# Kernel tuning notes

Measured on AMD Instinct MI355X. Metric: run time of the kernel, lower is better.

The kernel has to match this reference:

```python
import jax, jax.numpy as jnp
import numpy as np

EPS_NORM = 1e-08
EPS_Q = 1e-05

def rmsnorm(x, w):
    v = jnp.mean(jnp.square(x.astype(jnp.float32)), axis=-1, keepdims=True)
    x_hat = x * jax.lax.rsqrt(v + EPS_NORM)
    return (x_hat * w).astype(x.dtype)

def activation_quant(x):
    # per-token 8-bit fake quant
    scale = 127.0 / jnp.clip(jnp.max(jnp.abs(x), axis=-1, keepdims=True), EPS_Q, None)
    return jnp.clip(jnp.round(x * scale), -128, 127) / scale

def weight_quant(w):
    # per-tensor 1.58-bit (ternary) fake quant
    scale = 1.0 / jnp.clip(jnp.mean(jnp.abs(w)), EPS_Q, None)
    return jnp.clip(jnp.round(w * scale), -1, 1) / scale

def bitlinear(x, norm_w, w):
    x_norm = rmsnorm(x, norm_w)
    x_q = x_norm + jax.lax.stop_gradient(activation_quant(x_norm) - x_norm)
    w_q = w + jax.lax.stop_gradient(weight_quant(w) - w)
    return jnp.einsum('bsd,hd->bsh', x_q, w_q)

def setup_inputs() -> dict:
    key = jax.random.key(0)
    k1, k2, k3 = jax.random.split(key, 3)
    dim, hidden = 1024, 4096
    return {
        'x': jax.random.normal(k1, (4, 2048, dim), dtype=jnp.float32),
        'norm1_w': jnp.ones((dim,), jnp.float32),
        'w1': jax.random.normal(k2, (hidden, dim), jnp.float32) * 0.02,
        'act_scale': jnp.ones((1,), jnp.float32),
        'act_bias': jnp.zeros((1,), jnp.float32),
        'norm2_w': jnp.ones((hidden,), jnp.float32),
        'w2': jax.random.normal(k3, (dim, hidden), jnp.float32) * 0.02,
    }

def reference(x, norm1_w, w1, act_scale, act_bias, norm2_w, w2):
    h = bitlinear(x, norm1_w, w1)                       # [B,S,hidden]
    h = act_scale * jnp.square(jax.nn.relu(h)) + act_bias  # StarReLU
    y = bitlinear(h, norm2_w, w2)                       # [B,S,dim]
    return y
```

## Files before the change

### kernel.cpp

```cpp
#include <hip/hip_runtime.h>
#include <stdint.h>

#define EPS_NORM 1e-8
#define EPS_Q 1e-5

typedef int v4i __attribute__((ext_vector_type(4)));

__device__ __forceinline__ double wave_sum_d(double v) {
#pragma unroll
  for (int o = 32; o; o >>= 1) v += __shfl_xor(v, o);
  return v;
}
__device__ __forceinline__ float wave_max(float v) {
#pragma unroll
  for (int o = 32; o; o >>= 1) v = fmaxf(v, __shfl_xor(v, o));
  return v;
}

__global__ void wabs_sum_kernel(const float* __restrict__ w1,
                                const float* __restrict__ w2,
                                double* __restrict__ sums) {
  const float4* w = (const float4*)(blockIdx.y ? w2 : w1);
  const int n4 = 4194304 / 4;
  double s = 0.0;
  for (int i = blockIdx.x * blockDim.x + threadIdx.x; i < n4;
       i += gridDim.x * blockDim.x) {
    float4 t = w[i];
    s += (double)fabsf(t.x) + (double)fabsf(t.y) + (double)fabsf(t.z) +
         (double)fabsf(t.w);
  }
  s = wave_sum_d(s);
  __shared__ double red[4];
  const int wid = threadIdx.x >> 6;
  if ((threadIdx.x & 63) == 0) red[wid] = s;
  __syncthreads();
  if (threadIdx.x == 0)
    atomicAdd(&sums[blockIdx.y], red[0] + red[1] + red[2] + red[3]);
}

__global__ void wquant_kernel(const float* __restrict__ w, int8_t* __restrict__ q,
                              const double* __restrict__ sum, double ninv) {
  const double s = 1.0 / fmax(sum[0] * ninv, EPS_Q);
  const int i = blockIdx.x * blockDim.x + threadIdx.x;
  float4 t = ((const float4*)w)[i];
  int a = (int)rint((double)t.x * s); a = a < -1 ? -1 : (a > 1 ? 1 : a);
  int b = (int)rint((double)t.y * s); b = b < -1 ? -1 : (b > 1 ? 1 : b);
  int c = (int)rint((double)t.z * s); c = c < -1 ? -1 : (c > 1 ? 1 : c);
  int d = (int)rint((double)t.w * s); d = d < -1 ? -1 : (d > 1 ? 1 : d);
  ((int*)q)[i] = (a & 255) | ((b & 255) << 8) | ((c & 255) << 16) | ((d & 255) << 24);
}

template <int D>
__global__ __launch_bounds__(256) void rq_kernel(
    const float* __restrict__ X, const float* __restrict__ W,
    int8_t* __restrict__ Q, float* __restrict__ recips) {
  constexpr int C = D / 1024;
  const int t = blockIdx.x;
  const int tid = threadIdx.x;
  const int wid = tid >> 6;
  const int lane = tid & 63;
  const float4* xr = (const float4*)(X + (size_t)t * D);
  const float4* wr = (const float4*)W;
  float4 xv[C];
  double ss = 0.0;
#pragma unroll
  for (int c = 0; c < C; ++c) {
    xv[c] = xr[c * 256 + tid];
    ss += (double)xv[c].x * xv[c].x + (double)xv[c].y * xv[c].y +
          (double)xv[c].z * xv[c].z + (double)xv[c].w * xv[c].w;
  }
  ss = wave_sum_d(ss);
  __shared__ double reds[4];
  __shared__ float redm[4];
  if (lane == 0) reds[wid] = ss;
  __syncthreads();
  const double v = (reds[0] + reds[1] + reds[2] + reds[3]) * (1.0 / (double)D);
  const float rs = (float)(1.0 / sqrt(v + EPS_NORM));
  float am = 0.f;
#pragma unroll
  for (int c = 0; c < C; ++c) {
    float4 wv = wr[c * 256 + tid];
    xv[c].x = (xv[c].x * rs) * wv.x;
    xv[c].y = (xv[c].y * rs) * wv.y;
    xv[c].z = (xv[c].z * rs) * wv.z;
    xv[c].w = (xv[c].w * rs) * wv.w;
    am = fmaxf(am, fmaxf(fmaxf(fabsf(xv[c].x), fabsf(xv[c].y)),
                         fmaxf(fabsf(xv[c].z), fabsf(xv[c].w))));
  }
  am = wave_max(am);
  if (lane == 0) redm[wid] = am;
  __syncthreads();
  am = fmaxf(fmaxf(redm[0], redm[1]), fmaxf(redm[2], redm[3]));
  am = fmaxf(am, 1e-5f);
  const float scale = 127.f / am;
  int8_t* qrow = Q + (size_t)t * D;
#pragma unroll
  for (int c = 0; c < C; ++c) {
    int q0 = (int)rintf(xv[c].x * scale); q0 = q0 < -128 ? -128 : (q0 > 127 ? 127 : q0);
    int q1 = (int)rintf(xv[c].y * scale); q1 = q1 < -128 ? -128 : (q1 > 127 ? 127 : q1);
    int q2 = (int)rintf(xv[c].z * scale); q2 = q2 < -128 ? -128 : (q2 > 127 ? 127 : q2);
    int q3 = (int)rintf(xv[c].w * scale); q3 = q3 < -128 ? -128 : (q3 > 127 ? 127 : q3);
    ((int*)qrow)[c * 256 + tid] =
        (q0 & 255) | ((q1 & 255) << 8) | ((q2 & 255) << 16) | ((q3 & 255) << 24);
  }
  if (tid == 0) recips[t] = am * (1.f / 127.f);
}

template <bool STAR>
__global__ __launch_bounds__(256) void gemm_i8_kernel(
    const int8_t* __restrict__ A, const int8_t* __restrict__ B,
    float* __restrict__ C, int N, int K, const float* __restrict__ tokrecip,
    const double* __restrict__ wsum, double wninv,
    const float* __restrict__ sa_p, const float* __restrict__ sb_p) {
  __shared__ int8_t smem[32768];
  int8_t* As = smem;
  int8_t* Bs = smem + 16384;
  const int tid = threadIdx.x;
  const int lane = tid & 63;
  const int wid = tid >> 6;
  const int n0 = blockIdx.x * 128;
  const int t0 = blockIdx.y * 128;

  const int srow = tid >> 3;
  const int scol = ((tid & 7) ^ (srow & 7)) << 4;
  const int8_t* Ag = A + (size_t)(t0 + srow) * K + scol;
  const int8_t* Bg = B + (size_t)(n0 + srow) * K + scol;

  v4i acc[4][4];
  v4i zero = {0, 0, 0, 0};
#pragma unroll
  for (int m = 0; m < 4; ++m)
#pragma unroll
    for (int n = 0; n < 4; ++n) acc[m][n] = zero;

  const int wr = (wid >> 1) << 6;
  const int wc = (wid & 1) << 6;
  const int fr = lane & 15;
  const int fk = (lane >> 4) << 4;

  for (int k0 = 0; k0 < K; k0 += 128) {
#pragma unroll
    for (int j = 0; j < 4; ++j) {
      __builtin_amdgcn_global_load_lds(
          (const __attribute__((address_space(1))) void*)(Ag + (size_t)(j * 32) * K + k0),
          (__attribute__((address_space(3))) void*)(As + j * 4096 + wid * 1024),
          16, 0, 0);
      __builtin_amdgcn_global_load_lds(
          (const __attribute__((address_space(1))) void*)(Bg + (size_t)(j * 32) * K + k0),
          (__attribute__((address_space(3))) void*)(Bs + j * 4096 + wid * 1024),
          16, 0, 0);
    }
    __syncthreads();
#pragma unroll
    for (int kk = 0; kk < 2; ++kk) {
      v4i a[4], b[4];
#pragma unroll
      for (int m = 0; m < 4; ++m) {
        const int row = wr + m * 16 + fr;
        const int col = (kk * 64 + fk) ^ ((row & 7) << 4);
        a[m] = *(const v4i*)(As + row * 128 + col);
      }
#pragma unroll
      for (int n = 0; n < 4; ++n) {
        const int row = wc + n * 16 + fr;
        const int col = (kk * 64 + fk) ^ ((row & 7) << 4);
        b[n] = *(const v4i*)(Bs + row * 128 + col);
      }
#pragma unroll
      for (int m = 0; m < 4; ++m)
#pragma unroll
        for (int n = 0; n < 4; ++n)
          acc[m][n] = __builtin_amdgcn_mfma_i32_16x16x64_i8(a[m], b[n], acc[m][n], 0, 0, 0);
    }
    __syncthreads();
  }

  const float wrecip = (float)fmax(wsum[0] * wninv, EPS_Q);
  float sa = 0.f, sb = 0.f;
  if (STAR) { sa = sa_p[0]; sb = sb_p[0]; }
  const int r0 = t0 + wr + ((lane >> 4) << 2);
  const int c0 = n0 + wc + (lane & 15);
#pragma unroll
  for (int m = 0; m < 4; ++m) {
    float tr[4];
#pragma unroll
    for (int r = 0; r < 4; ++r) tr[r] = tokrecip[r0 + m * 16 + r] * wrecip;
#pragma unroll
    for (int n = 0; n < 4; ++n) {
#pragma unroll
      for (int r = 0; r < 4; ++r) {
        float f = (float)acc[m][n][r] * tr[r];
        if (STAR) {
          const float rl = fmaxf(f, 0.f);
          f = fmaf(sa, rl * rl, sb);
        }
        C[(size_t)(r0 + m * 16 + r) * N + (c0 + n * 16)] = f;
      }
    }
  }
}

extern "C" void kernel_launch(void* const* d_in, const int* in_sizes, int n_in,
                              void* d_out, int out_size, void* d_ws, size_t ws_size,
                              hipStream_t stream) {
  const float* x    = (const float*)d_in[0];
  const float* n1w  = (const float*)d_in[1];
  const float* w1   = (const float*)d_in[2];
  const float* as_p = (const float*)d_in[3];
  const float* ab_p = (const float*)d_in[4];
  const float* n2w  = (const float*)d_in[5];
  const float* w2   = (const float*)d_in[6];
  float* out = (float*)d_out;

  char* ws = (char*)d_ws;
  float*  h   = (float*)ws;
  int8_t* x1q = (int8_t*)(ws + 134217728ULL);
  int8_t* x2q = (int8_t*)(ws + 134217728ULL);
  int8_t* w1q = (int8_t*)(ws + 167772160ULL);
  int8_t* w2q = (int8_t*)(ws + 171966464ULL);
  float*  tr1 = (float*)(ws + 176160768ULL);
  float*  tr2 = (float*)(ws + 176193536ULL);
  double* sums = (double*)(ws + 176226304ULL);

  hipMemsetAsync(sums, 0, 2 * sizeof(double), stream);
  wabs_sum_kernel<<<dim3(512, 2), 256, 0, stream>>>(w1, w2, sums);
  wquant_kernel<<<4096, 256, 0, stream>>>(w1, w1q, sums + 0, 1.0 / 4194304.0);
  wquant_kernel<<<4096, 256, 0, stream>>>(w2, w2q, sums + 1, 1.0 / 4194304.0);
  rq_kernel<1024><<<8192, 256, 0, stream>>>(x, n1w, x1q, tr1);
  gemm_i8_kernel<true><<<dim3(32, 64), 256, 0, stream>>>(
      x1q, w1q, h, 4096, 1024, tr1, sums + 0, 1.0 / 4194304.0, as_p, ab_p);
  rq_kernel<4096><<<8192, 256, 0, stream>>>(h, n2w, x2q, tr2);
  gemm_i8_kernel<false><<<dim3(8, 64), 256, 0, stream>>>(
      x2q, w2q, out, 1024, 4096, tr2, sums + 1, 1.0 / 4194304.0, nullptr, nullptr);
}
```

Before: 263.6 us.

## Drop memset and atomics for weight sums, merge wquant launches, narrow second GEMM tile

```diff
diff --git a/kernel.cpp b/kernel.cpp
--- a/kernel.cpp
+++ b/kernel.cpp
@@ -19,7 +19,7 @@
 
 __global__ void wabs_sum_kernel(const float* __restrict__ w1,
                                 const float* __restrict__ w2,
-                                double* __restrict__ sums) {
+                                double* __restrict__ partials) {
   const float4* w = (const float4*)(blockIdx.y ? w2 : w1);
   const int n4 = 4194304 / 4;
   double s = 0.0;
@@ -35,18 +35,29 @@
   if ((threadIdx.x & 63) == 0) red[wid] = s;
   __syncthreads();
   if (threadIdx.x == 0)
-    atomicAdd(&sums[blockIdx.y], red[0] + red[1] + red[2] + red[3]);
-}
-
-__global__ void wquant_kernel(const float* __restrict__ w, int8_t* __restrict__ q,
-                              const double* __restrict__ sum, double ninv) {
-  const double s = 1.0 / fmax(sum[0] * ninv, EPS_Q);
+    partials[blockIdx.y * 512 + blockIdx.x] = red[0] + red[1] + red[2] + red[3];
+}
+
+__global__ void wquant_kernel(const float* __restrict__ w1,
+                              const float* __restrict__ w2,
+                              int8_t* __restrict__ q1, int8_t* __restrict__ q2,
+                              const double* __restrict__ partials) {
+  const int tz = blockIdx.y;
+  const float* w = tz ? w2 : w1;
+  int8_t* q = tz ? q2 : q1;
+  double s = partials[tz * 512 + threadIdx.x] + partials[tz * 512 + 256 + threadIdx.x];
+  s = wave_sum_d(s);
+  __shared__ double red[4];
+  if ((threadIdx.x & 63) == 0) red[threadIdx.x >> 6] = s;
+  __syncthreads();
+  const double total = red[0] + red[1] + red[2] + red[3];
+  const double sc = 1.0 / fmax(total * (1.0 / 4194304.0), EPS_Q);
   const int i = blockIdx.x * blockDim.x + threadIdx.x;
   float4 t = ((const float4*)w)[i];
-  int a = (int)rint((double)t.x * s); a = a < -1 ? -1 : (a > 1 ? 1 : a);
-  int b = (int)rint((double)t.y * s); b = b < -1 ? -1 : (b > 1 ? 1 : b);
-  int c = (int)rint((double)t.z * s); c = c < -1 ? -1 : (c > 1 ? 1 : c);
-  int d = (int)rint((double)t.w * s); d = d < -1 ? -1 : (d > 1 ? 1 : d);
+  int a = (int)rint((double)t.x * sc); a = a < -1 ? -1 : (a > 1 ? 1 : a);
+  int b = (int)rint((double)t.y * sc); b = b < -1 ? -1 : (b > 1 ? 1 : b);
+  int c = (int)rint((double)t.z * sc); c = c < -1 ? -1 : (c > 1 ? 1 : c);
+  int d = (int)rint((double)t.w * sc); d = d < -1 ? -1 : (d > 1 ? 1 : d);
   ((int*)q)[i] = (a & 255) | ((b & 255) << 8) | ((c & 255) << 16) | ((d & 255) << 24);
 }
 
@@ -106,87 +117,95 @@
   if (tid == 0) recips[t] = am * (1.f / 127.f);
 }
 
-template <bool STAR>
+template <int MF, int NF, bool STAR>
 __global__ __launch_bounds__(256) void gemm_i8_kernel(
     const int8_t* __restrict__ A, const int8_t* __restrict__ B,
     float* __restrict__ C, int N, int K, const float* __restrict__ tokrecip,
-    const double* __restrict__ wsum, double wninv,
+    const double* __restrict__ partials, double wninv,
     const float* __restrict__ sa_p, const float* __restrict__ sb_p) {
-  __shared__ int8_t smem[32768];
+  constexpr int MT = MF * 32;
+  constexpr int NT = NF * 32;
+  __shared__ int8_t smem[(MT + NT) * 128];
   int8_t* As = smem;
-  int8_t* Bs = smem + 16384;
+  int8_t* Bs = smem + MT * 128;
   const int tid = threadIdx.x;
   const int lane = tid & 63;
   const int wid = tid >> 6;
-  const int n0 = blockIdx.x * 128;
-  const int t0 = blockIdx.y * 128;
+  const int n0 = blockIdx.x * NT;
+  const int t0 = blockIdx.y * MT;
+
+  double wsum = 0.0;
+#pragma unroll 8
+  for (int i = lane; i < 512; i += 64) wsum += partials[i + (STAR ? 0 : 512)];
+  wsum = wave_sum_d(wsum);
+  const float wrecip = (float)fmax(wsum * wninv, EPS_Q);
 
   const int srow = tid >> 3;
   const int scol = ((tid & 7) ^ (srow & 7)) << 4;
   const int8_t* Ag = A + (size_t)(t0 + srow) * K + scol;
   const int8_t* Bg = B + (size_t)(n0 + srow) * K + scol;
 
-  v4i acc[4][4];
+  v4i acc[MF][NF];
   v4i zero = {0, 0, 0, 0};
 #pragma unroll
-  for (int m = 0; m < 4; ++m)
-#pragma unroll
-    for (int n = 0; n < 4; ++n) acc[m][n] = zero;
-
-  const int wr = (wid >> 1) << 6;
-  const int wc = (wid & 1) << 6;
+  for (int m = 0; m < MF; ++m)
+#pragma unroll
+    for (int n = 0; n < NF; ++n) acc[m][n] = zero;
+
+  const int wr = (wid >> 1) * (MF * 16);
+  const int wc = (wid & 1) * (NF * 16);
   const int fr = lane & 15;
   const int fk = (lane >> 4) << 4;
 
   for (int k0 = 0; k0 < K; k0 += 128) {
 #pragma unroll
-    for (int j = 0; j < 4; ++j) {
+    for (int j = 0; j < MF; ++j)
       __builtin_amdgcn_global_load_lds(
           (const __attribute__((address_space(1))) void*)(Ag + (size_t)(j * 32) * K + k0),
           (__attribute__((address_space(3))) void*)(As + j * 4096 + wid * 1024),
           16, 0, 0);
+#pragma unroll
+    for (int j = 0; j < NF; ++j)
       __builtin_amdgcn_global_load_lds(
           (const __attribute__((address_space(1))) void*)(Bg + (size_t)(j * 32) * K + k0),
           (__attribute__((address_space(3))) void*)(Bs + j * 4096 + wid * 1024),
           16, 0, 0);
-    }
     __syncthreads();
 #pragma unroll
     for (int kk = 0; kk < 2; ++kk) {
-      v4i a[4], b[4];
-#pragma unroll
-      for (int m = 0; m < 4; ++m) {
+      v4i a[MF], b[NF];
+#pragma unroll
+      for (int m = 0; m < MF; ++m) {
         const int row = wr + m * 16 + fr;
         const int col = (kk * 64 + fk) ^ ((row & 7) << 4);
         a[m] = *(const v4i*)(As + row * 128 + col);
       }
 #pragma unroll
-      for (int n = 0; n < 4; ++n) {
+      for (int n = 0; n < NF; ++n) {
         const int row = wc + n * 16 + fr;
         const int col = (kk * 64 + fk) ^ ((row & 7) << 4);
         b[n] = *(const v4i*)(Bs + row * 128 + col);
       }
 #pragma unroll
-      for (int m = 0; m < 4; ++m)
-#pragma unroll
-        for (int n = 0; n < 4; ++n)
+      for (int m = 0; m < MF; ++m)
+#pragma unroll
+        for (int n = 0; n < NF; ++n)
           acc[m][n] = __builtin_amdgcn_mfma_i32_16x16x64_i8(a[m], b[n], acc[m][n], 0, 0, 0);
     }
     __syncthreads();
   }
 
-  const float wrecip = (float)fmax(wsum[0] * wninv, EPS_Q);
   float sa = 0.f, sb = 0.f;
   if (STAR) { sa = sa_p[0]; sb = sb_p[0]; }
   const int r0 = t0 + wr + ((lane >> 4) << 2);
   const int c0 = n0 + wc + (lane & 15);
 #pragma unroll
-  for (int m = 0; m < 4; ++m) {
+  for (int m = 0; m < MF; ++m) {
     float tr[4];
 #pragma unroll
     for (int r = 0; r < 4; ++r) tr[r] = tokrecip[r0 + m * 16 + r] * wrecip;
 #pragma unroll
-    for (int n = 0; n < 4; ++n) {
+    for (int n = 0; n < NF; ++n) {
 #pragma unroll
       for (int r = 0; r < 4; ++r) {
         float f = (float)acc[m][n][r] * tr[r];
@@ -220,16 +239,14 @@
   int8_t* w2q = (int8_t*)(ws + 171966464ULL);
   float*  tr1 = (float*)(ws + 176160768ULL);
   float*  tr2 = (float*)(ws + 176193536ULL);
-  double* sums = (double*)(ws + 176226304ULL);
-
-  hipMemsetAsync(sums, 0, 2 * sizeof(double), stream);
-  wabs_sum_kernel<<<dim3(512, 2), 256, 0, stream>>>(w1, w2, sums);
-  wquant_kernel<<<4096, 256, 0, stream>>>(w1, w1q, sums + 0, 1.0 / 4194304.0);
-  wquant_kernel<<<4096, 256, 0, stream>>>(w2, w2q, sums + 1, 1.0 / 4194304.0);
+  double* partials = (double*)(ws + 176226304ULL);
+
+  wabs_sum_kernel<<<dim3(512, 2), 256, 0, stream>>>(w1, w2, partials);
+  wquant_kernel<<<dim3(4096, 2), 256, 0, stream>>>(w1, w2, w1q, w2q, partials);
   rq_kernel<1024><<<8192, 256, 0, stream>>>(x, n1w, x1q, tr1);
-  gemm_i8_kernel<true><<<dim3(32, 64), 256, 0, stream>>>(
-      x1q, w1q, h, 4096, 1024, tr1, sums + 0, 1.0 / 4194304.0, as_p, ab_p);
+  gemm_i8_kernel<4, 4, true><<<dim3(32, 64), 256, 0, stream>>>(
+      x1q, w1q, h, 4096, 1024, tr1, partials, 1.0 / 4194304.0, as_p, ab_p);
   rq_kernel<4096><<<8192, 256, 0, stream>>>(h, n2w, x2q, tr2);
-  gemm_i8_kernel<false><<<dim3(8, 64), 256, 0, stream>>>(
-      x2q, w2q, out, 1024, 4096, tr2, sums + 1, 1.0 / 4194304.0, nullptr, nullptr);
-}
+  gemm_i8_kernel<4, 2, false><<<dim3(16, 64), 256, 0, stream>>>(
+      x2q, w2q, out, 1024, 4096, tr2, partials, 1.0 / 4194304.0, nullptr, nullptr);
+}
```

After: 251.0 us. 4.8% less time.
